# Kernel tuning notes

Hardware: AMD Instinct MI355X
Metric: run time of the kernel (lower is better)

Reference implementation:

```python
import jax, jax.numpy as jnp
import numpy as np

N_TOTAL_USERS = 200000
N_TOTAL_ITEMS = 300000
N_DOM_USERS = 60000
N_DOM_ITEMS = 90000
N_DOMAINS = 3
DIM = 32           # hidden_dim // 2
N_LAYERS = 2
ALPHA = 0.1


def grec_conv(src, dst, x, n_nodes):
    """LightGCN-style propagation with APPNP residual (alpha), symmetric norm.
    Edge dropout is disabled (eval mode). x: [n_nodes, d]."""
    ones = jnp.ones(src.shape[0], dtype=x.dtype)
    deg = jax.ops.segment_sum(ones, dst, num_segments=n_nodes)
    inv_sqrt = jax.lax.rsqrt(jnp.maximum(deg, 1.0))
    w = inv_sqrt[src] * inv_sqrt[dst]            # [E] edge norm
    h = x
    for _ in range(N_LAYERS):
        msg = h[src] * w[:, None]                # gather + scale, [E, d]
        agg = jax.ops.segment_sum(msg, dst, num_segments=n_nodes)
        h = (1.0 - ALPHA) * agg + ALPHA * x      # residual to layer-0 emb
    return h


def setup_inputs() -> dict:
    key = jax.random.key(0)
    ks = jax.random.split(key, 8)
    return {
        "dom_edges": jax.random.randint(ks[0], (2, 2000000), 0, N_DOM_USERS + N_DOM_ITEMS, dtype=jnp.int32),
        "sep_edges": jax.random.randint(ks[1], (3, 2, 2000000), 0, N_TOTAL_USERS + N_TOTAL_ITEMS, dtype=jnp.int32),
        "aggr_user_w": 0.1 * jax.random.normal(ks[2], (N_TOTAL_USERS, DIM), dtype=jnp.float32),
        "aggr_item_w": 0.1 * jax.random.normal(ks[3], (N_TOTAL_ITEMS, DIM), dtype=jnp.float32),
        "dom_user_w": 0.1 * jax.random.normal(ks[4], (N_DOM_USERS, DIM), dtype=jnp.float32),
        "dom_item_w": 0.1 * jax.random.normal(ks[5], (N_DOM_ITEMS, DIM), dtype=jnp.float32),
        "user_ids_dom": jnp.arange(N_DOM_USERS, dtype=jnp.int32),
        "item_ids_dom": jnp.arange(N_DOM_ITEMS, dtype=jnp.int32),
        "users": jax.random.randint(ks[6], (8192,), 0, N_DOM_USERS).astype(jnp.int64),
        "items": jax.random.randint(ks[7], (8192,), 0, N_DOM_ITEMS).astype(jnp.int64),
    }


def reference(dom_edges, sep_edges, aggr_user_w, aggr_item_w,
              dom_user_w, dom_item_w, user_ids_dom, item_ids_dom,
              users, items):
    n_dom_nodes = N_DOM_USERS + N_DOM_ITEMS
    n_all_nodes = N_TOTAL_USERS + N_TOTAL_ITEMS

    # ---- intra-domain conv (mode='dis_intra') on the domain graph ----
    x_intra = jnp.concatenate([dom_user_w, dom_item_w], axis=0)
    h_intra = grec_conv(dom_edges[0], dom_edges[1], x_intra, n_dom_nodes)
    user_intra = h_intra[:N_DOM_USERS]
    item_intra = h_intra[N_DOM_USERS:]

    # ---- inter-domain conv (mode='dis_inter'): per-domain sep graphs, mean ----
    x_inter = jnp.concatenate([aggr_user_w, aggr_item_w], axis=0)
    embs = []
    for d in range(N_DOMAINS):  # small fixed loop over domains
        h = grec_conv(sep_edges[d, 0], sep_edges[d, 1], x_inter, n_all_nodes)
        uss = h[:N_TOTAL_USERS][user_ids_dom]   # gather this domain's users
        its = h[N_TOTAL_USERS:][item_ids_dom]   # gather this domain's items
        embs.append(jnp.concatenate([uss, its], axis=0))
    light_out = jnp.mean(jnp.stack(embs, axis=1), axis=1)  # [n_dom_nodes, DIM]
    user_inter = light_out[:N_DOM_USERS]
    item_inter = light_out[N_DOM_USERS:]

    # ---- concat inter || intra, score query pairs ----
    all_users = jnp.concatenate([user_inter, user_intra], axis=1)  # [Nu_d, 64]
    all_items = jnp.concatenate([item_inter, item_intra], axis=1)
    users_emb = all_users[users]
    items_emb = all_items[items]
    gamma = jnp.sum(users_emb * items_emb, axis=1)  # [B]
    return gamma
```

## Files before the change

kernel.cpp:

```cpp
#include <hip/hip_runtime.h>


static constexpr int NTU = 200000, NTI = 300000, NDU = 60000, NDI = 90000;
static constexpr int NDOMN = 150000, NALLN = 500000, NE = 2000000;
static constexpr int DIM = 32, NQ = 8192;
static constexpr int TN = NDOMN + 3 * NALLN;

static constexpr int BSH_I = 9,  BN_I = 512,  NBK_I = 293, CAP_I = 7680;
static constexpr int BSH_E = 11, BN_E = 2048, NBK_E = 245, CAP_E = 9216;
static constexpr int GEW_I = NBK_I * CAP_I;
static constexpr int GEW_E = NBK_E * CAP_E;
static constexpr int GEW   = GEW_I + 3 * GEW_E;
static constexpr int NBCK  = NBK_I + 3 * NBK_E;
static constexpr int ACT_CAP = 360000;
static constexpr int BLKP = 512;
static constexpr int PCHUNK = 8192;
static constexpr int PBLK_PG = (NE + PCHUNK - 1) / PCHUNK;

static constexpr size_t a256(size_t x) { return (x + 255) & ~(size_t)255; }
static constexpr size_t O_NEED  = 0;
static constexpr size_t O_N1    = a256((size_t)NDOMN * 4);
static constexpr size_t ZB      = O_N1 + a256(TN);
static constexpr size_t O_RANK  = ZB;
static constexpr size_t O_BSUM  = O_RANK + a256((size_t)NDOMN * 4);
static constexpr size_t O_BCUR  = O_BSUM + 1024;
static constexpr size_t O_DEG8  = O_BCUR + a256(NBCK * 4);
static constexpr size_t O_OFF   = O_DEG8 + a256(TN);
static constexpr size_t O_RANK1 = O_OFF  + a256((size_t)TN * 4);
static constexpr size_t O_ALIST = O_RANK1 + a256((size_t)TN * 4);
static constexpr size_t O_NLIST = O_ALIST + a256((size_t)ACT_CAP * 4);
static constexpr size_t O_GE    = O_NLIST + a256((size_t)16384 * 4);
static constexpr size_t O_AGG1  = O_GE   + (size_t)GEW * 4;
static constexpr size_t O_A2    = O_AGG1 + (size_t)ACT_CAP * DIM * 4;

__device__ __forceinline__ unsigned blockScanIncl256(unsigned s, unsigned* wsum4, int t) {
    int lane = t & 63, wid = t >> 6;
    unsigned x = s;
    #pragma unroll
    for (int o = 1; o < 64; o <<= 1) {
        unsigned y = __shfl_up(x, o);
        if (lane >= o) x += y;
    }
    if (lane == 63) wsum4[wid] = x;
    __syncthreads();
    unsigned wo = 0;
    if (wid > 0) wo += wsum4[0];
    if (wid > 1) wo += wsum4[1];
    if (wid > 2) wo += wsum4[2];
    return x + wo;
}

__global__ void k_setup(uint4* __restrict__ zp, int n16, unsigned* __restrict__ bcur) {
    int t = blockIdx.x * blockDim.x + threadIdx.x;
    if (t < n16) zp[t] = make_uint4(0u, 0u, 0u, 0u);
    if (t < NBCK) {
        int g, b;
        if (t < NBK_I) { g = 0; b = t; }
        else { int r = t - NBK_I; g = 1 + r / NBK_E; b = r - (g - 1) * NBK_E; }
        unsigned geb = (g == 0) ? 0u : (unsigned)(GEW_I + (g - 1) * GEW_E);
        unsigned cap = (g == 0) ? CAP_I : CAP_E;
        bcur[t] = geb + (unsigned)b * cap;
    }
}

__global__ void k_scatter_needed(const int* __restrict__ users, const int* __restrict__ items,
                                 unsigned* __restrict__ need) {
    int t = blockIdx.x * blockDim.x + threadIdx.x;
    if (t < NQ)            need[users[t]] = 1u;
    else if (t < 2 * NQ)   need[NDU + items[t - NQ]] = 1u;
}

__global__ __launch_bounds__(BLKP, 4) void k_part(const int* __restrict__ dom,
                                                  const int* __restrict__ sep,
                                                  unsigned* __restrict__ bcur,
                                                  unsigned* __restrict__ gE) {
    __shared__ unsigned hist[512], gbase[512];
    int t = threadIdx.x;
    int g = blockIdx.x / PBLK_PG;
    int chunk = blockIdx.x - g * PBLK_PG;
    const int* src = (g == 0) ? dom : sep + (size_t)(g - 1) * 2 * NE;
    const int* dst = src + NE;
    int bsh = (g == 0) ? BSH_I : BSH_E;
    unsigned bnm = (g == 0) ? (BN_I - 1) : (BN_E - 1);
    int nbk = (g == 0) ? NBK_I : NBK_E;
    unsigned cap = (g == 0) ? CAP_I : CAP_E;
    unsigned geb = (g == 0) ? 0u : (unsigned)(GEW_I + (g - 1) * GEW_E);
    int bco = (g == 0) ? 0 : NBK_I + (g - 1) * NBK_E;
    hist[t] = 0u;
    __syncthreads();
    int vbase = chunk * (PCHUNK / 4);
    unsigned pk[16], bp[16];
    #pragma unroll
    for (int i = 0; i < 4; i++) {
        int vi = vbase + i * BLKP + t;
        if (vi < NE / 4) {
            int4 sv = ((const int4*)src)[vi];
            int4 dv = ((const int4*)dst)[vi];
            int ss[4] = {sv.x, sv.y, sv.z, sv.w};
            int dd[4] = {dv.x, dv.y, dv.z, dv.w};
            #pragma unroll
            for (int e = 0; e < 4; e++) {
                unsigned d = (unsigned)dd[e];
                unsigned b = d >> bsh;
                unsigned p = atomicAdd(&hist[b], 1u);
                pk[i * 4 + e] = ((d & bnm) << 19) | (unsigned)ss[e];
                bp[i * 4 + e] = (b << 13) | p;
            }
        } else {
            #pragma unroll
            for (int e = 0; e < 4; e++) bp[i * 4 + e] = 0xFFFFFFFFu;
        }
    }
    __syncthreads();
    if (t < nbk) {
        unsigned c = hist[t];
        if (c) {
            unsigned gb = atomicAdd(&bcur[bco + t], c);
            gbase[t] = (gb + c <= geb + (unsigned)(t + 1) * cap) ? gb : 0xFFFFFFFFu;
        }
    }
    __syncthreads();
    #pragma unroll
    for (int i = 0; i < 16; i++) {
        unsigned bpv = bp[i];
        if (bpv != 0xFFFFFFFFu) {
            unsigned b = bpv >> 13, p = bpv & 8191u;
            unsigned gb = gbase[b];
            if (gb != 0xFFFFFFFFu) gE[gb + p] = pk[i];
        }
    }
}

__global__ __launch_bounds__(256) void k_sortb(unsigned* __restrict__ gE,
                                               const unsigned* __restrict__ bcur,
                                               unsigned* __restrict__ off,
                                               unsigned char* __restrict__ deg8) {
    __shared__ unsigned ed[CAP_E];
    __shared__ unsigned h2[BN_E];
    __shared__ unsigned wsum4[4];
    int t = threadIdx.x, bx = blockIdx.x;
    int g, b;
    if (bx < NBK_I) { g = 0; b = bx; }
    else { int r = bx - NBK_I; g = 1 + r / NBK_E; b = r - (g - 1) * NBK_E; }
    int bn = (g == 0) ? BN_I : BN_E;
    unsigned cap = (g == 0) ? CAP_I : CAP_E;
    unsigned geb = (g == 0) ? 0u : (unsigned)(GEW_I + (g - 1) * GEW_E);
    int bco = (g == 0) ? 0 : NBK_I + (g - 1) * NBK_E;
    int nb = (g == 0) ? 0 : NDOMN + (g - 1) * NALLN;
    int nnodes = (g == 0) ? NDOMN : NALLN;
    unsigned j0 = geb + (unsigned)b * cap;
    unsigned cnt = bcur[bco + b] - j0;
    if (cnt > cap) cnt = cap;
    for (unsigned j = t; j < cnt; j += 256) ed[j] = gE[j0 + j];
    for (int k = t; k < bn; k += 256) h2[k] = 0u;
    __syncthreads();
    for (unsigned j = t; j < cnt; j += 256) atomicAdd(&h2[ed[j] >> 19], 1u);
    __syncthreads();
    int E = bn >> 8;
    unsigned c[8], pre[8]; unsigned ssum = 0;
    int k0 = t * E;
    for (int q = 0; q < E; q++) { c[q] = h2[k0 + q]; pre[q] = ssum; ssum += c[q]; }
    unsigned x = blockScanIncl256(ssum, wsum4, t);
    unsigned excl = x - ssum;
    int vb = b * bn;
    for (int q = 0; q < E; q++) {
        int v = vb + k0 + q;
        if (v < nnodes) { off[nb + v] = j0 + excl + pre[q]; deg8[nb + v] = (unsigned char)c[q]; }
    }
    for (int q = 0; q < E; q++) h2[k0 + q] = excl + pre[q];
    __syncthreads();
    for (unsigned j = t; j < cnt; j += 256) {
        unsigned e = ed[j];
        unsigned p = atomicAdd(&h2[e >> 19], 1u);
        gE[j0 + p] = e & 0x7FFFFu;
    }
}

__global__ void k_mark(const unsigned* __restrict__ nlist, const unsigned* __restrict__ off,
                       const unsigned char* __restrict__ deg8, const unsigned* __restrict__ gE,
                       unsigned char* __restrict__ n1) {
    int t = blockIdx.x * blockDim.x + threadIdx.x;
    if (t >= 4 * 16384) return;
    int r = t >> 2, g = t & 3;
    unsigned v = nlist[r];
    if (v >= (unsigned)NDOMN) return;
    int nb, node;
    if (g == 0) { nb = 0; node = (int)v; }
    else { nb = NDOMN + (g - 1) * NALLN; node = ((int)v < NDU) ? (int)v : NTU + ((int)v - NDU); }
    int gv = nb + node;
    unsigned j0 = off[gv];
    int dg = deg8[gv];
    unsigned char* n1g = n1 + nb;
    for (int j = 0; j < dg; j++) n1g[gE[j0 + j]] = 1;
}

static constexpr int SCAN_T = 256;

template <int EL, typename T>
__global__ void k_scan1(const T* __restrict__ in, unsigned* __restrict__ out,
                        unsigned* __restrict__ bsum, int n) {
    __shared__ unsigned wsum4[4];
    int b = blockIdx.x, t = threadIdx.x;
    int base = b * (SCAN_T * EL) + t * EL;
    unsigned v[EL]; unsigned s = 0;
    for (int i = 0; i < EL; i++) { int idx = base + i; v[i] = (idx < n) ? (unsigned)in[idx] : 0u; s += v[i]; }
    unsigned x = blockScanIncl256(s, wsum4, t);
    unsigned running = x - s;
    for (int i = 0; i < EL; i++) { int idx = base + i; if (idx < n) out[idx] = running; running += v[i]; }
    if (t == SCAN_T - 1) bsum[b] = x;
}

template <int CH>
__global__ void k_scan3n(unsigned* __restrict__ rank, const unsigned* __restrict__ bsum,
                         const unsigned* __restrict__ need, unsigned* __restrict__ nlist,
                         int n, int nbv) {
    __shared__ unsigned wsum4[4];
    __shared__ unsigned sb[SCAN_T];
    int t = threadIdx.x;
    unsigned s = (t < nbv) ? bsum[t] : 0u;
    unsigned x = blockScanIncl256(s, wsum4, t);
    sb[t] = x - s;
    __syncthreads();
    int i = blockIdx.x * blockDim.x + t;
    if (i < n) {
        unsigned r = rank[i] + sb[i / CH];
        rank[i] = r;
        if (need[i]) nlist[r] = (unsigned)i;
    }
}

template <int CH>
__global__ void k_scan3f(unsigned* __restrict__ rank1, const unsigned* __restrict__ bsum,
                         const unsigned char* __restrict__ n1, unsigned* __restrict__ alist,
                         int n, int nbv) {
    __shared__ unsigned wsum4[4];
    __shared__ unsigned sb[SCAN_T];
    int t = threadIdx.x;
    unsigned s = (t < nbv) ? bsum[t] : 0u;
    unsigned x = blockScanIncl256(s, wsum4, t);
    sb[t] = x - s;
    __syncthreads();
    int i = blockIdx.x * blockDim.x + t;
    if (i < n) {
        unsigned r = rank1[i] + sb[i / CH];
        rank1[i] = r;
        if (n1[i] && r < ACT_CAP) alist[r] = (unsigned)i;
    }
}

__global__ __launch_bounds__(256) void k_gather1(const unsigned* __restrict__ alist,
                          const unsigned* __restrict__ off,
                          const unsigned char* __restrict__ deg8, const unsigned* __restrict__ gE,
                          const float* __restrict__ auw, const float* __restrict__ aiw,
                          const float* __restrict__ duw, const float* __restrict__ diw,
                          float* __restrict__ agg1) {
    int t = blockIdx.x * blockDim.x + threadIdx.x;
    int r = t >> 3, c = t & 7;
    if (r >= ACT_CAP) return;
    unsigned gv = alist[r];
    if (gv >= (unsigned)TN) return;
    int g, nb;
    if ((int)gv < NDOMN) { g = 0; nb = 0; }
    else { int q = (int)gv - NDOMN; g = 1 + q / NALLN; nb = NDOMN + (g - 1) * NALLN; }
    int v = (int)gv - nb;
    const float* uw = g ? auw : duw;
    const float* iw = g ? aiw : diw;
    int UB = g ? NTU : NDU;
    const unsigned char* d8 = deg8 + nb;
    unsigned j0 = off[gv];
    int dg = deg8[gv];
    float invd = rsqrtf(fmaxf((float)dg, 1.0f));
    float4 acc = make_float4(0.f, 0.f, 0.f, 0.f);
    int j = 0;
    for (; j + 8 <= dg; j += 8) {
        int s_[8];
        #pragma unroll
        for (int k = 0; k < 8; k++) s_[k] = (int)gE[j0 + j + k];
        float w_[8];
        #pragma unroll
        for (int k = 0; k < 8; k++) w_[k] = rsqrtf(fmaxf((float)d8[s_[k]], 1.0f)) * invd;
        #pragma unroll
        for (int k = 0; k < 8; k++) {
            float4 xv = ((const float4*)((s_[k] < UB) ? uw + (size_t)s_[k] * DIM
                                                      : iw + (size_t)(s_[k] - UB) * DIM))[c];
            acc.x += w_[k] * xv.x; acc.y += w_[k] * xv.y;
            acc.z += w_[k] * xv.z; acc.w += w_[k] * xv.w;
        }
    }
    for (; j + 4 <= dg; j += 4) {
        int s0 = (int)gE[j0 + j], s1 = (int)gE[j0 + j + 1];
        int s2 = (int)gE[j0 + j + 2], s3 = (int)gE[j0 + j + 3];
        float4 x0 = ((const float4*)((s0 < UB) ? uw + (size_t)s0 * DIM : iw + (size_t)(s0 - UB) * DIM))[c];
        float4 x1 = ((const float4*)((s1 < UB) ? uw + (size_t)s1 * DIM : iw + (size_t)(s1 - UB) * DIM))[c];
        float4 x2 = ((const float4*)((s2 < UB) ? uw + (size_t)s2 * DIM : iw + (size_t)(s2 - UB) * DIM))[c];
        float4 x3 = ((const float4*)((s3 < UB) ? uw + (size_t)s3 * DIM : iw + (size_t)(s3 - UB) * DIM))[c];
        float w0 = rsqrtf(fmaxf((float)d8[s0], 1.0f)) * invd;
        float w1 = rsqrtf(fmaxf((float)d8[s1], 1.0f)) * invd;
        float w2 = rsqrtf(fmaxf((float)d8[s2], 1.0f)) * invd;
        float w3 = rsqrtf(fmaxf((float)d8[s3], 1.0f)) * invd;
        acc.x += w0 * x0.x + w1 * x1.x + w2 * x2.x + w3 * x3.x;
        acc.y += w0 * x0.y + w1 * x1.y + w2 * x2.y + w3 * x3.y;
        acc.z += w0 * x0.z + w1 * x1.z + w2 * x2.z + w3 * x3.z;
        acc.w += w0 * x0.w + w1 * x1.w + w2 * x2.w + w3 * x3.w;
    }
    for (; j < dg; j++) {
        int s = (int)gE[j0 + j];
        float w = rsqrtf(fmaxf((float)d8[s], 1.0f)) * invd;
        float4 xv = ((const float4*)((s < UB) ? uw + (size_t)s * DIM : iw + (size_t)(s - UB) * DIM))[c];
        acc.x += w * xv.x; acc.y += w * xv.y; acc.z += w * xv.z; acc.w += w * xv.w;
    }
    float4 xo = ((const float4*)((v < UB) ? uw + (size_t)v * DIM : iw + (size_t)(v - UB) * DIM))[c];
    float4 A;
    A.x = 0.9f * acc.x + 0.1f * xo.x;
    A.y = 0.9f * acc.y + 0.1f * xo.y;
    A.z = 0.9f * acc.z + 0.1f * xo.z;
    A.w = 0.9f * acc.w + 0.1f * xo.w;
    ((float4*)(agg1 + (size_t)r * DIM))[c] = A;
}

__global__ __launch_bounds__(256) void k_gather2(const unsigned* __restrict__ nlist,
                          const unsigned* __restrict__ rank,
                          const unsigned* __restrict__ rank1, const unsigned* __restrict__ off,
                          const unsigned char* __restrict__ deg8, const unsigned* __restrict__ gE,
                          const float* __restrict__ agg1, float* __restrict__ a2) {
    int t = blockIdx.x * blockDim.x + threadIdx.x;
    int idx = t >> 3, c = t & 7;
    int g = idx >> 14;
    int r = idx & 16383;
    unsigned v = nlist[r];
    if (v >= (unsigned)NDOMN) return;
    int nb, node;
    if (g == 0) { nb = 0; node = (int)v; }
    else { nb = NDOMN + (g - 1) * NALLN; node = ((int)v < NDU) ? (int)v : NTU + ((int)v - NDU); }
    int gv = nb + node;
    unsigned j0 = off[gv];
    int dg = deg8[gv];
    float invd = rsqrtf(fmaxf((float)dg, 1.0f));
    const unsigned char* d8 = deg8 + nb;
    const unsigned* r1 = rank1 + nb;
    float4 acc = make_float4(0.f, 0.f, 0.f, 0.f);
    int j = 0;
    for (; j + 8 <= dg; j += 8) {
        int s_[8];
        #pragma unroll
        for (int k = 0; k < 8; k++) s_[k] = (int)gE[j0 + j + k];
        unsigned ar_[8]; float w_[8];
        #pragma unroll
        for (int k = 0; k < 8; k++) {
            ar_[k] = r1[s_[k]];
            w_[k] = rsqrtf(fmaxf((float)d8[s_[k]], 1.0f)) * invd;
        }
        #pragma unroll
        for (int k = 0; k < 8; k++) {
            float4 A = ((const float4*)(agg1 + (size_t)ar_[k] * DIM))[c];
            acc.x += w_[k] * A.x; acc.y += w_[k] * A.y;
            acc.z += w_[k] * A.z; acc.w += w_[k] * A.w;
        }
    }
    for (; j + 4 <= dg; j += 4) {
        int s0 = (int)gE[j0 + j], s1 = (int)gE[j0 + j + 1];
        int s2 = (int)gE[j0 + j + 2], s3 = (int)gE[j0 + j + 3];
        unsigned a0 = r1[s0], a1 = r1[s1], a2i = r1[s2], a3 = r1[s3];
        float4 A0 = ((const float4*)(agg1 + (size_t)a0 * DIM))[c];
        float4 A1 = ((const float4*)(agg1 + (size_t)a1 * DIM))[c];
        float4 A2 = ((const float4*)(agg1 + (size_t)a2i * DIM))[c];
        float4 A3 = ((const float4*)(agg1 + (size_t)a3 * DIM))[c];
        float w0 = rsqrtf(fmaxf((float)d8[s0], 1.0f)) * invd;
        float w1 = rsqrtf(fmaxf((float)d8[s1], 1.0f)) * invd;
        float w2 = rsqrtf(fmaxf((float)d8[s2], 1.0f)) * invd;
        float w3 = rsqrtf(fmaxf((float)d8[s3], 1.0f)) * invd;
        acc.x += w0 * A0.x + w1 * A1.x + w2 * A2.x + w3 * A3.x;
        acc.y += w0 * A0.y + w1 * A1.y + w2 * A2.y + w3 * A3.y;
        acc.z += w0 * A0.z + w1 * A1.z + w2 * A2.z + w3 * A3.z;
        acc.w += w0 * A0.w + w1 * A1.w + w2 * A2.w + w3 * A3.w;
    }
    for (; j < dg; j++) {
        int s = (int)gE[j0 + j];
        unsigned ar = r1[s];
        float w = rsqrtf(fmaxf((float)d8[s], 1.0f)) * invd;
        float4 A = ((const float4*)(agg1 + (size_t)ar * DIM))[c];
        acc.x += w * A.x; acc.y += w * A.y; acc.z += w * A.z; acc.w += w * A.w;
    }
    ((float4*)(a2 + ((size_t)g * 16384 + rank[v]) * DIM))[c] = acc;
}

__global__ void k_gamma(const int* __restrict__ users, const int* __restrict__ items,
                        const unsigned* __restrict__ rank, const float* __restrict__ a2,
                        const float* __restrict__ auw, const float* __restrict__ aiw,
                        const float* __restrict__ duw, const float* __restrict__ diw,
                        float* __restrict__ out) {
    int t = blockIdx.x * blockDim.x + threadIdx.x;
    int q = t >> 3;
    if (q >= NQ) return;
    int c = t & 7;
    int u = users[q], it = items[q];
    int ru = (int)rank[u], ri = (int)rank[NDU + it];
    auto A2 = [&](int g, int r) { return ((const float4*)(a2 + ((size_t)g * 16384 + r) * DIM))[c]; };
    float4 Du = A2(0, ru), Di = A2(0, ri);
    float4 U1 = A2(1, ru), U2 = A2(2, ru), U3 = A2(3, ru);
    float4 V1 = A2(1, ri), V2 = A2(2, ri), V3 = A2(3, ri);
    float4 xu = ((const float4*)(auw + (size_t)u * DIM))[c];
    float4 xi = ((const float4*)(aiw + (size_t)it * DIM))[c];
    float4 yu = ((const float4*)(duw + (size_t)u * DIM))[c];
    float4 yi = ((const float4*)(diw + (size_t)it * DIM))[c];
    float s = 0.f;
    s += (0.3f * (U1.x + U2.x + U3.x) + 0.1f * xu.x) * (0.3f * (V1.x + V2.x + V3.x) + 0.1f * xi.x);
    s += (0.3f * (U1.y + U2.y + U3.y) + 0.1f * xu.y) * (0.3f * (V1.y + V2.y + V3.y) + 0.1f * xi.y);
    s += (0.3f * (U1.z + U2.z + U3.z) + 0.1f * xu.z) * (0.3f * (V1.z + V2.z + V3.z) + 0.1f * xi.z);
    s += (0.3f * (U1.w + U2.w + U3.w) + 0.1f * xu.w) * (0.3f * (V1.w + V2.w + V3.w) + 0.1f * xi.w);
    s += (0.9f * Du.x + 0.1f * yu.x) * (0.9f * Di.x + 0.1f * yi.x);
    s += (0.9f * Du.y + 0.1f * yu.y) * (0.9f * Di.y + 0.1f * yi.y);
    s += (0.9f * Du.z + 0.1f * yu.z) * (0.9f * Di.z + 0.1f * yi.z);
    s += (0.9f * Du.w + 0.1f * yu.w) * (0.9f * Di.w + 0.1f * yi.w);
    s += __shfl_xor(s, 1);
    s += __shfl_xor(s, 2);
    s += __shfl_xor(s, 4);
    if (c == 0) out[q] = s;
}

extern "C" void kernel_launch(void* const* d_in, const int* in_sizes, int n_in,
                              void* d_out, int out_size, void* d_ws, size_t ws_size,
                              hipStream_t stream) {
    const int*   dom_edges = (const int*)d_in[0];
    const int*   sep_edges = (const int*)d_in[1];
    const float* auw       = (const float*)d_in[2];
    const float* aiw       = (const float*)d_in[3];
    const float* duw       = (const float*)d_in[4];
    const float* diw       = (const float*)d_in[5];
    const int*   users     = (const int*)d_in[8];
    const int*   items     = (const int*)d_in[9];
    float*       out       = (float*)d_out;

    char* ws = (char*)d_ws;
    unsigned*      need  = (unsigned*)(ws + O_NEED);
    unsigned char* n1    = (unsigned char*)(ws + O_N1);
    unsigned*      rank  = (unsigned*)(ws + O_RANK);
    unsigned*      bsum  = (unsigned*)(ws + O_BSUM);
    unsigned*      bcur  = (unsigned*)(ws + O_BCUR);
    unsigned char* deg8  = (unsigned char*)(ws + O_DEG8);
    unsigned*      off   = (unsigned*)(ws + O_OFF);
    unsigned*      rank1 = (unsigned*)(ws + O_RANK1);
    unsigned*      alist = (unsigned*)(ws + O_ALIST);
    unsigned*      nlist = (unsigned*)(ws + O_NLIST);
    unsigned*      gE    = (unsigned*)(ws + O_GE);
    float*         agg1  = (float*)(ws + O_AGG1);
    float*         a2    = (float*)(ws + O_A2);

    const int BLK = 256;
    auto cdiv = [](long a, long b) { return (int)((a + b - 1) / b); };

    int n16 = (int)(ZB / 16);
    k_setup<<<cdiv(n16, BLK), BLK, 0, stream>>>((uint4*)ws, n16, bcur);
    k_scatter_needed<<<cdiv(2 * NQ, BLK), BLK, 0, stream>>>(users, items, need);

    {
        int nbv = cdiv(NDOMN, SCAN_T * 8);
        k_scan1<8, unsigned><<<nbv, SCAN_T, 0, stream>>>(need, rank, bsum, NDOMN);
        k_scan3n<SCAN_T * 8><<<cdiv(NDOMN, BLK), BLK, 0, stream>>>(rank, bsum, need, nlist,
                                                                   NDOMN, nbv);
    }

    k_part<<<4 * PBLK_PG, BLKP, 0, stream>>>(dom_edges, sep_edges, bcur, gE);

    k_sortb<<<NBCK, 256, 0, stream>>>(gE, bcur, off, deg8);

    k_mark<<<cdiv((long)4 * 16384, BLK), BLK, 0, stream>>>(nlist, off, deg8, gE, n1);

    {
        int nbv = cdiv(TN, SCAN_T * 32);
        k_scan1<32, unsigned char><<<nbv, SCAN_T, 0, stream>>>(n1, rank1, bsum, TN);
        k_scan3f<SCAN_T * 32><<<cdiv(TN, BLK), BLK, 0, stream>>>(rank1, bsum, n1, alist,
                                                                 TN, nbv);
    }

    k_gather1<<<cdiv((long)ACT_CAP * 8, BLK), BLK, 0, stream>>>(alist, off, deg8, gE,
                                                                auw, aiw, duw, diw, agg1);
    k_gather2<<<cdiv((long)4 * 16384 * 8, BLK), BLK, 0, stream>>>(nlist, rank, rank1, off, deg8,
                                                                  gE, agg1, a2);

    k_gamma<<<cdiv((long)NQ * 8, BLK), BLK, 0, stream>>>(users, items, rank, a2,
                                                         auw, aiw, duw, diw, out);
}
```

Before: 376.3 us.

## Fuse setup, scan and mark kernels into cooperative kernels with grid sync

```diff
diff --git a/kernel.cpp b/kernel.cpp
--- a/kernel.cpp
+++ b/kernel.cpp
@@ -1,4 +1,7 @@
 #include <hip/hip_runtime.h>
+#include <hip/hip_cooperative_groups.h>
+
+namespace cg = cooperative_groups;
 
 
 static constexpr int NTU = 200000, NTI = 300000, NDU = 60000, NDI = 90000;
@@ -16,6 +19,9 @@
 static constexpr int BLKP = 512;
 static constexpr int PCHUNK = 8192;
 static constexpr int PBLK_PG = (NE + PCHUNK - 1) / PCHUNK;
+static constexpr int SCAN_T = 256;
+static constexpr int NTILES_NEED = (NDOMN + SCAN_T * 8 - 1) / (SCAN_T * 8);
+static constexpr int NTILES_N1   = (TN + SCAN_T * 32 - 1) / (SCAN_T * 32);
 
 static constexpr size_t a256(size_t x) { return (x + 255) & ~(size_t)255; }
 static constexpr size_t O_NEED  = 0;
@@ -50,24 +56,64 @@
     return x + wo;
 }
 
-__global__ void k_setup(uint4* __restrict__ zp, int n16, unsigned* __restrict__ bcur) {
-    int t = blockIdx.x * blockDim.x + threadIdx.x;
-    if (t < n16) zp[t] = make_uint4(0u, 0u, 0u, 0u);
-    if (t < NBCK) {
-        int g, b;
-        if (t < NBK_I) { g = 0; b = t; }
-        else { int r = t - NBK_I; g = 1 + r / NBK_E; b = r - (g - 1) * NBK_E; }
-        unsigned geb = (g == 0) ? 0u : (unsigned)(GEW_I + (g - 1) * GEW_E);
-        unsigned cap = (g == 0) ? CAP_I : CAP_E;
-        bcur[t] = geb + (unsigned)b * cap;
-    }
-}
-
-__global__ void k_scatter_needed(const int* __restrict__ users, const int* __restrict__ items,
-                                 unsigned* __restrict__ need) {
-    int t = blockIdx.x * blockDim.x + threadIdx.x;
-    if (t < NQ)            need[users[t]] = 1u;
-    else if (t < 2 * NQ)   need[NDU + items[t - NQ]] = 1u;
+__global__ __launch_bounds__(256, 4) void k_pre(const int* __restrict__ users,
+                                                const int* __restrict__ items,
+                                                char* __restrict__ ws) {
+    __shared__ unsigned wsum4[4];
+    __shared__ unsigned sb[SCAN_T];
+    unsigned* need  = (unsigned*)(ws + O_NEED);
+    unsigned* rank  = (unsigned*)(ws + O_RANK);
+    unsigned* bsum  = (unsigned*)(ws + O_BSUM);
+    unsigned* bcur  = (unsigned*)(ws + O_BCUR);
+    unsigned* nlist = (unsigned*)(ws + O_NLIST);
+    cg::grid_group grid = cg::this_grid();
+    int t = threadIdx.x;
+    int gid = blockIdx.x * 256 + t;
+    int NT = gridDim.x * 256;
+
+    {
+        uint4* zp = (uint4*)ws;
+        int n16 = (int)(ZB / 16);
+        for (int i = gid; i < n16; i += NT) zp[i] = make_uint4(0u, 0u, 0u, 0u);
+        for (int i = gid; i < NBCK; i += NT) {
+            int g, b;
+            if (i < NBK_I) { g = 0; b = i; }
+            else { int r = i - NBK_I; g = 1 + r / NBK_E; b = r - (g - 1) * NBK_E; }
+            unsigned geb = (g == 0) ? 0u : (unsigned)(GEW_I + (g - 1) * GEW_E);
+            unsigned cap = (g == 0) ? CAP_I : CAP_E;
+            bcur[i] = geb + (unsigned)b * cap;
+        }
+    }
+    grid.sync();
+    for (int i = gid; i < 2 * NQ; i += NT) {
+        if (i < NQ) need[users[i]] = 1u;
+        else        need[NDU + items[i - NQ]] = 1u;
+    }
+    grid.sync();
+    for (int w = blockIdx.x; w < NTILES_NEED; w += gridDim.x) {
+        __syncthreads();
+        int base = w * (SCAN_T * 8) + t * 8;
+        unsigned v[8]; unsigned s = 0;
+        #pragma unroll
+        for (int i = 0; i < 8; i++) { int idx = base + i; v[i] = (idx < NDOMN) ? need[idx] : 0u; s += v[i]; }
+        unsigned x = blockScanIncl256(s, wsum4, t);
+        unsigned running = x - s;
+        #pragma unroll
+        for (int i = 0; i < 8; i++) { int idx = base + i; if (idx < NDOMN) rank[idx] = running; running += v[i]; }
+        if (t == SCAN_T - 1) bsum[w] = x;
+    }
+    grid.sync();
+    {
+        unsigned s = (t < NTILES_NEED) ? bsum[t] : 0u;
+        unsigned x = blockScanIncl256(s, wsum4, t);
+        sb[t] = x - s;
+        __syncthreads();
+        for (int i = gid; i < NDOMN; i += NT) {
+            unsigned r = rank[i] + sb[i >> 11];
+            rank[i] = r;
+            if (need[i]) nlist[r] = (unsigned)i;
+        }
+    }
 }
 
 __global__ __launch_bounds__(BLKP, 4) void k_part(const int* __restrict__ dom,
@@ -176,75 +222,59 @@
     }
 }
 
-__global__ void k_mark(const unsigned* __restrict__ nlist, const unsigned* __restrict__ off,
-                       const unsigned char* __restrict__ deg8, const unsigned* __restrict__ gE,
-                       unsigned char* __restrict__ n1) {
-    int t = blockIdx.x * blockDim.x + threadIdx.x;
-    if (t >= 4 * 16384) return;
-    int r = t >> 2, g = t & 3;
-    unsigned v = nlist[r];
-    if (v >= (unsigned)NDOMN) return;
-    int nb, node;
-    if (g == 0) { nb = 0; node = (int)v; }
-    else { nb = NDOMN + (g - 1) * NALLN; node = ((int)v < NDU) ? (int)v : NTU + ((int)v - NDU); }
-    int gv = nb + node;
-    unsigned j0 = off[gv];
-    int dg = deg8[gv];
-    unsigned char* n1g = n1 + nb;
-    for (int j = 0; j < dg; j++) n1g[gE[j0 + j]] = 1;
-}
-
-static constexpr int SCAN_T = 256;
-
-template <int EL, typename T>
-__global__ void k_scan1(const T* __restrict__ in, unsigned* __restrict__ out,
-                        unsigned* __restrict__ bsum, int n) {
-    __shared__ unsigned wsum4[4];
-    int b = blockIdx.x, t = threadIdx.x;
-    int base = b * (SCAN_T * EL) + t * EL;
-    unsigned v[EL]; unsigned s = 0;
-    for (int i = 0; i < EL; i++) { int idx = base + i; v[i] = (idx < n) ? (unsigned)in[idx] : 0u; s += v[i]; }
-    unsigned x = blockScanIncl256(s, wsum4, t);
-    unsigned running = x - s;
-    for (int i = 0; i < EL; i++) { int idx = base + i; if (idx < n) out[idx] = running; running += v[i]; }
-    if (t == SCAN_T - 1) bsum[b] = x;
-}
-
-template <int CH>
-__global__ void k_scan3n(unsigned* __restrict__ rank, const unsigned* __restrict__ bsum,
-                         const unsigned* __restrict__ need, unsigned* __restrict__ nlist,
-                         int n, int nbv) {
+__global__ __launch_bounds__(256, 4) void k_post(char* __restrict__ ws) {
     __shared__ unsigned wsum4[4];
     __shared__ unsigned sb[SCAN_T];
+    unsigned char* n1    = (unsigned char*)(ws + O_N1);
+    unsigned char* deg8  = (unsigned char*)(ws + O_DEG8);
+    unsigned* off   = (unsigned*)(ws + O_OFF);
+    unsigned* rank1 = (unsigned*)(ws + O_RANK1);
+    unsigned* bsum  = (unsigned*)(ws + O_BSUM);
+    unsigned* alist = (unsigned*)(ws + O_ALIST);
+    unsigned* nlist = (unsigned*)(ws + O_NLIST);
+    unsigned* gE    = (unsigned*)(ws + O_GE);
+    cg::grid_group grid = cg::this_grid();
     int t = threadIdx.x;
-    unsigned s = (t < nbv) ? bsum[t] : 0u;
-    unsigned x = blockScanIncl256(s, wsum4, t);
-    sb[t] = x - s;
-    __syncthreads();
-    int i = blockIdx.x * blockDim.x + t;
-    if (i < n) {
-        unsigned r = rank[i] + sb[i / CH];
-        rank[i] = r;
-        if (need[i]) nlist[r] = (unsigned)i;
-    }
-}
-
-template <int CH>
-__global__ void k_scan3f(unsigned* __restrict__ rank1, const unsigned* __restrict__ bsum,
-                         const unsigned char* __restrict__ n1, unsigned* __restrict__ alist,
-                         int n, int nbv) {
-    __shared__ unsigned wsum4[4];
-    __shared__ unsigned sb[SCAN_T];
-    int t = threadIdx.x;
-    unsigned s = (t < nbv) ? bsum[t] : 0u;
-    unsigned x = blockScanIncl256(s, wsum4, t);
-    sb[t] = x - s;
-    __syncthreads();
-    int i = blockIdx.x * blockDim.x + t;
-    if (i < n) {
-        unsigned r = rank1[i] + sb[i / CH];
-        rank1[i] = r;
-        if (n1[i] && r < ACT_CAP) alist[r] = (unsigned)i;
+    int gid = blockIdx.x * 256 + t;
+    int NT = gridDim.x * 256;
+
+    for (int i = gid; i < 4 * 16384; i += NT) {
+        int r = i >> 2, g4 = i & 3;
+        unsigned v = nlist[r];
+        if (v >= (unsigned)NDOMN) continue;
+        int nb_, node;
+        if (g4 == 0) { nb_ = 0; node = (int)v; }
+        else { nb_ = NDOMN + (g4 - 1) * NALLN; node = ((int)v < NDU) ? (int)v : NTU + ((int)v - NDU); }
+        int gv = nb_ + node;
+        unsigned j0 = off[gv];
+        int dg = deg8[gv];
+        unsigned char* n1g = n1 + nb_;
+        for (int j = 0; j < dg; j++) n1g[gE[j0 + j]] = 1;
+    }
+    grid.sync();
+    for (int w = blockIdx.x; w < NTILES_N1; w += gridDim.x) {
+        __syncthreads();
+        int base = w * (SCAN_T * 32) + t * 32;
+        unsigned v[32]; unsigned s = 0;
+        #pragma unroll
+        for (int i = 0; i < 32; i++) { int idx = base + i; v[i] = (idx < TN) ? (unsigned)n1[idx] : 0u; s += v[i]; }
+        unsigned x = blockScanIncl256(s, wsum4, t);
+        unsigned running = x - s;
+        #pragma unroll
+        for (int i = 0; i < 32; i++) { int idx = base + i; if (idx < TN) rank1[idx] = running; running += v[i]; }
+        if (t == SCAN_T - 1) bsum[w] = x;
+    }
+    grid.sync();
+    {
+        unsigned s = (t < NTILES_N1) ? bsum[t] : 0u;
+        unsigned x = blockScanIncl256(s, wsum4, t);
+        sb[t] = x - s;
+        __syncthreads();
+        for (int i = gid; i < TN; i += NT) {
+            unsigned r = rank1[i] + sb[i >> 13];
+            rank1[i] = r;
+            if (n1[i] && r < ACT_CAP) alist[r] = (unsigned)i;
+        }
     }
 }
 
@@ -432,10 +462,7 @@
     float*       out       = (float*)d_out;
 
     char* ws = (char*)d_ws;
-    unsigned*      need  = (unsigned*)(ws + O_NEED);
-    unsigned char* n1    = (unsigned char*)(ws + O_N1);
     unsigned*      rank  = (unsigned*)(ws + O_RANK);
-    unsigned*      bsum  = (unsigned*)(ws + O_BSUM);
     unsigned*      bcur  = (unsigned*)(ws + O_BCUR);
     unsigned char* deg8  = (unsigned char*)(ws + O_DEG8);
     unsigned*      off   = (unsigned*)(ws + O_OFF);
@@ -449,28 +476,30 @@
     const int BLK = 256;
     auto cdiv = [](long a, long b) { return (int)((a + b - 1) / b); };
 
-    int n16 = (int)(ZB / 16);
-    k_setup<<<cdiv(n16, BLK), BLK, 0, stream>>>((uint4*)ws, n16, bcur);
-    k_scatter_needed<<<cdiv(2 * NQ, BLK), BLK, 0, stream>>>(users, items, need);
+    static int gridPre = 0, gridPost = 0;
+    if (gridPre == 0) {
+        int nb = 0;
+        hipOccupancyMaxActiveBlocksPerMultiprocessor(&nb, k_pre, 256, 0);
+        gridPre = (nb > 0 ? nb : 1) * 256;
+        if (gridPre > 1024) gridPre = 1024;
+        nb = 0;
+        hipOccupancyMaxActiveBlocksPerMultiprocessor(&nb, k_post, 256, 0);
+        gridPost = (nb > 0 ? nb : 1) * 256;
+        if (gridPost > 1024) gridPost = 1024;
+    }
 
     {
-        int nbv = cdiv(NDOMN, SCAN_T * 8);
-        k_scan1<8, unsigned><<<nbv, SCAN_T, 0, stream>>>(need, rank, bsum, NDOMN);
-        k_scan3n<SCAN_T * 8><<<cdiv(NDOMN, BLK), BLK, 0, stream>>>(rank, bsum, need, nlist,
-                                                                   NDOMN, nbv);
+        void* args[] = { (void*)&users, (void*)&items, (void*)&ws };
+        hipLaunchCooperativeKernel(k_pre, dim3(gridPre), dim3(256), args, 0, stream);
     }
 
     k_part<<<4 * PBLK_PG, BLKP, 0, stream>>>(dom_edges, sep_edges, bcur, gE);
 
     k_sortb<<<NBCK, 256, 0, stream>>>(gE, bcur, off, deg8);
 
-    k_mark<<<cdiv((long)4 * 16384, BLK), BLK, 0, stream>>>(nlist, off, deg8, gE, n1);
-
     {
-        int nbv = cdiv(TN, SCAN_T * 32);
-        k_scan1<32, unsigned char><<<nbv, SCAN_T, 0, stream>>>(n1, rank1, bsum, TN);
-        k_scan3f<SCAN_T * 32><<<cdiv(TN, BLK), BLK, 0, stream>>>(rank1, bsum, n1, alist,
-                                                                 TN, nbv);
+        void* args[] = { (void*)&ws };
+        hipLaunchCooperativeKernel(k_post, dim3(gridPost), dim3(256), args, 0, stream);
     }
 
     k_gather1<<<cdiv((long)ACT_CAP * 8, BLK), BLK, 0, stream>>>(alist, off, deg8, gE,
```

Result: slower. 772.5 us (+105.3%).
